# Kernel optimization log

Measured on AMD Instinct MI355X. Metric: run time of the kernel, lower is better.

The kernel has to match this reference:

```python
import jax, jax.numpy as jnp
import numpy as np

D_MODEL = 1024
N_HEAD = 16
D_HEAD = D_MODEL // N_HEAD
SEQ = 1024
RLEN = 2 * SEQ
BATCH = 4
LN_EPS = 1e-5


def setup_inputs() -> dict:
    key = jax.random.key(0)
    ks = jax.random.split(key, 12)
    s = 0.02
    return {
        "h": jax.random.normal(ks[0], (SEQ, BATCH, D_MODEL), jnp.float32),
        "r": jax.random.normal(ks[1], (RLEN, BATCH, D_MODEL), jnp.float32),
        "q_w": jax.random.normal(ks[2], (D_MODEL, N_HEAD, D_HEAD), jnp.float32) * s,
        "k_w": jax.random.normal(ks[3], (D_MODEL, N_HEAD, D_HEAD), jnp.float32) * s,
        "v_w": jax.random.normal(ks[4], (D_MODEL, N_HEAD, D_HEAD), jnp.float32) * s,
        "o_w": jax.random.normal(ks[5], (D_MODEL, N_HEAD, D_HEAD), jnp.float32) * s,
        "r_w": jax.random.normal(ks[6], (D_MODEL, N_HEAD, D_HEAD), jnp.float32) * s,
        "r_r_bias": jax.random.normal(ks[7], (N_HEAD, D_HEAD), jnp.float32) * s,
        "r_w_bias": jax.random.normal(ks[8], (N_HEAD, D_HEAD), jnp.float32) * s,
        "ln_gamma": jnp.ones((D_MODEL,), jnp.float32),
        "ln_beta": jnp.zeros((D_MODEL,), jnp.float32),
    }


def rel_shift_bnij(x, klen):
    # x: [b, n, i, j]; Transformer-XL relative-shift trick
    b, n, i, j = x.shape
    x = x.reshape(b, n, j, i)[:, :, 1:, :].reshape(b, n, i, j - 1)
    return x[:, :, :, :klen]


def reference(h, r, q_w, k_w, v_w, o_w, r_w, r_r_bias, r_w_bias, ln_gamma, ln_beta):
    scale = 1.0 / np.sqrt(D_HEAD).astype(np.float32)
    # projections: i=seq, b=batch, n=heads, d=head dim
    q_head = jnp.einsum('ibh,hnd->ibnd', h, q_w)
    k_head = jnp.einsum('ibh,hnd->ibnd', h, k_w)
    v_head = jnp.einsum('ibh,hnd->ibnd', h, v_w)
    k_head_r = jnp.einsum('ibh,hnd->ibnd', r, r_w)
    # content and position attention scores
    ac = jnp.einsum('ibnd,jbnd->bnij', q_head + r_w_bias, k_head)
    bd = jnp.einsum('ibnd,jbnd->bnij', q_head + r_r_bias, k_head_r)
    bd = rel_shift_bnij(bd, klen=ac.shape[3])
    attn_prob = jax.nn.softmax((ac + bd) * scale, axis=3)  # dropout is identity at eval
    attn_vec = jnp.einsum('bnij,jbnd->ibnd', attn_prob, v_head)
    attn_out = jnp.einsum('ibnd,hnd->ibh', attn_vec, o_w) + h  # residual
    mu = jnp.mean(attn_out, axis=-1, keepdims=True)
    var = jnp.var(attn_out, axis=-1, keepdims=True)
    return (attn_out - mu) / jnp.sqrt(var + LN_EPS) * ln_gamma + ln_beta
```

## Files before the change

### kernel.cpp

```cpp
#include <hip/hip_runtime.h>
#include <stdint.h>


typedef __attribute__((ext_vector_type(8))) short v8s;
typedef __attribute__((ext_vector_type(4))) float v4f;

__device__ __forceinline__ uint16_t f2b(float x) {
    uint32_t u = __builtin_bit_cast(uint32_t, x);
    u += 0x7fffu + ((u >> 16) & 1u);
    return (uint16_t)(u >> 16);
}

__device__ __forceinline__ void gld16(const void* g, void* lds) {
    __builtin_amdgcn_global_load_lds(
        (const __attribute__((address_space(1))) uint32_t*)g,
        (__attribute__((address_space(3))) uint32_t*)lds, 16, 0, 0);
}

__global__ __launch_bounds__(256) void prep_kernel(
    const float* __restrict__ h, const float* __restrict__ r,
    const float* __restrict__ o_w, const float* __restrict__ q_w,
    const float* __restrict__ k_w, const float* __restrict__ v_w,
    const float* __restrict__ r_w,
    uint64_t* __restrict__ hB, uint64_t* __restrict__ rB,
    uint64_t* __restrict__ owB, uint16_t* __restrict__ Wcat,
    uint16_t* __restrict__ rwT)
{
    __shared__ float t[64][65];
    const int bid = blockIdx.x, tid = threadIdx.x;
    if (bid < 1024) {
        const int tx = bid & 15, ty = (bid >> 4) & 15, z = bid >> 8;
        const int n0 = tx * 64, h0 = ty * 64;
        const float* src = (z == 0) ? q_w : (z == 1) ? k_w : (z == 2) ? v_w : r_w;
        uint16_t* dst = (z == 3) ? rwT : Wcat + (size_t)z * 1048576;
#pragma unroll
        for (int q = 0; q < 16; ++q) {
            int idx = q * 256 + tid, rr = idx >> 6, cc = idx & 63;
            t[rr][cc] = src[(size_t)(h0 + rr) * 1024 + n0 + cc];
        }
        __syncthreads();
#pragma unroll
        for (int q = 0; q < 16; ++q) {
            int idx = q * 256 + tid, rr = idx >> 6, cc = idx & 63;
            dst[(size_t)(n0 + rr) * 1024 + h0 + cc] = f2b(t[cc][rr]);
        }
    } else {
        const float4* h4 = (const float4*)h;
        const float4* r4 = (const float4*)r;
        const float4* w4 = (const float4*)o_w;
        const int total = 1048576 + 2097152 + 262144;
        for (int i = (bid - 1024) * 256 + tid; i < total; i += 2048 * 256) {
            float4 v; uint64_t* dst; int idx;
            if (i < 1048576)      { idx = i;           v = h4[idx]; dst = hB; }
            else if (i < 3145728) { idx = i - 1048576; v = r4[idx]; dst = rB; }
            else                  { idx = i - 3145728; v = w4[idx]; dst = owB; }
            uint64_t p = (uint64_t)f2b(v.x) | ((uint64_t)f2b(v.y) << 16)
                       | ((uint64_t)f2b(v.z) << 32) | ((uint64_t)f2b(v.w) << 48);
            dst[idx] = p;
        }
    }
}

template<int MODE, int MI>
__device__ __forceinline__ void gemm_body(
    const uint16_t* __restrict__ A, const uint16_t* __restrict__ B, int K,
    int bx, int by, uint16_t* As, uint16_t* Bs,
    uint16_t* __restrict__ o0, uint16_t* __restrict__ o1,
    uint16_t* __restrict__ o2, uint16_t* __restrict__ o3,
    const float* __restrict__ bias0, const float* __restrict__ bias1,
    float* __restrict__ fo, const float* __restrict__ fres)
{
    const int tid = threadIdx.x;
    const int w = tid >> 6, lane = tid & 63;
    const int g = lane >> 4, c15 = lane & 15;
    const int m0 = by * (MI * 32), n0 = bx * 128;
    const int wr = w >> 1, wc = w & 1;

    int rowA[MI], colA[MI];
#pragma unroll
    for (int q = 0; q < MI; ++q) {
        int D = (w * MI + q) * 1024 + lane * 16;
        int row = D >> 7;
        rowA[q] = row;
        colA[q] = (D & 127) ^ ((row & 7) << 4);
    }
    int rowB[4], colB[4];
#pragma unroll
    for (int q = 0; q < 4; ++q) {
        int D = (w * 4 + q) * 1024 + lane * 16;
        int row = D >> 7;
        rowB[q] = row;
        colB[q] = (D & 127) ^ ((row & 7) << 4);
    }

    v4f acc[MI][4];
#pragma unroll
    for (int i = 0; i < MI; ++i)
#pragma unroll
        for (int j = 0; j < 4; ++j) acc[i][j] = v4f{0.f, 0.f, 0.f, 0.f};

    const char* Abase = (const char*)(A + (size_t)m0 * K);
    const char* Bbase = (const char*)(B + (size_t)n0 * K);
    const size_t ld = (size_t)K * 2;

    for (int kb = 0; kb < K; kb += 64) {
        if (kb) __syncthreads();
#pragma unroll
        for (int q = 0; q < MI; ++q)
            gld16(Abase + (size_t)rowA[q] * ld + (size_t)kb * 2 + colA[q],
                  (char*)As + (w * MI + q) * 1024);
#pragma unroll
        for (int q = 0; q < 4; ++q)
            gld16(Bbase + (size_t)rowB[q] * ld + (size_t)kb * 2 + colB[q],
                  (char*)Bs + (w * 4 + q) * 1024);
        asm volatile("s_waitcnt vmcnt(0)" ::: "memory");
        __syncthreads();

        v8s af[MI][2], bf[4][2];
#pragma unroll
        for (int mi = 0; mi < MI; ++mi) {
            int row = wr * (MI * 16) + mi * 16 + c15;
#pragma unroll
            for (int ks = 0; ks < 2; ++ks) {
                int cl = ks * 64 + g * 16;
                af[mi][ks] = *(const v8s*)((const char*)As + row * 128 + (cl ^ ((row & 7) << 4)));
            }
        }
#pragma unroll
        for (int ni = 0; ni < 4; ++ni) {
            int row = wc * 64 + ni * 16 + c15;
#pragma unroll
            for (int ks = 0; ks < 2; ++ks) {
                int cl = ks * 64 + g * 16;
                bf[ni][ks] = *(const v8s*)((const char*)Bs + row * 128 + (cl ^ ((row & 7) << 4)));
            }
        }
#pragma unroll
        for (int mi = 0; mi < MI; ++mi)
#pragma unroll
            for (int ni = 0; ni < 4; ++ni)
#pragma unroll
                for (int ks = 0; ks < 2; ++ks)
                    acc[mi][ni] = __builtin_amdgcn_mfma_f32_16x16x32_bf16(
                        af[mi][ks], bf[ni][ks], acc[mi][ni], 0, 0, 0);
    }

#pragma unroll
    for (int mi = 0; mi < MI; ++mi)
#pragma unroll
        for (int ni = 0; ni < 4; ++ni)
#pragma unroll
            for (int t = 0; t < 4; ++t) {
                int row = m0 + wr * (MI * 16) + mi * 16 + g * 4 + t;
                int col = n0 + wc * 64 + ni * 16 + c15;
                float v = acc[mi][ni][t];
                if (MODE == 0) {
                    int seg = col >> 10, nd = col & 1023;
                    int i = row >> 2, b = row & 3, n = nd >> 6, d = nd & 63;
                    int bn = b * 16 + n;
                    if (seg == 0) {
                        o0[(bn << 16) + (i << 6) + d] = f2b(v + bias0[nd]);
                        o1[(bn << 16) + (i << 6) + d] = f2b(v + bias1[nd]);
                    } else if (seg == 1) {
                        o2[(bn << 16) + (i << 6) + d] = f2b(v);
                    } else {
                        int il = i & 63;
                        int iperm = (i & ~63) | ((il & 15) * 4 + (il >> 4));
                        o3[(bn << 16) + (d << 10) + iperm] = f2b(v);
                    }
                } else if (MODE == 1) {
                    int j = row >> 2, b = row & 3, n = col >> 6, d = col & 63;
                    int bn = b * 16 + n;
                    o0[(bn << 17) + (j << 6) + d] = f2b(v);
                } else {
                    size_t idx = (size_t)row * 1024 + col;
                    fo[idx] = v + fres[idx];
                }
            }
}

__global__ __launch_bounds__(256) void gemm_qkvr(
    const uint16_t* __restrict__ hB, const uint16_t* __restrict__ Wcat,
    const uint16_t* __restrict__ rB, const uint16_t* __restrict__ rwT,
    uint16_t* __restrict__ Qw, uint16_t* __restrict__ Qr,
    uint16_t* __restrict__ Kt, uint16_t* __restrict__ Vt,
    uint16_t* __restrict__ Kr,
    const float* __restrict__ b0, const float* __restrict__ b1)
{
    __shared__ __align__(16) uint16_t As[128 * 64];
    __shared__ __align__(16) uint16_t Bs[128 * 64];
    const int bid = blockIdx.x;
    if (bid < 768) {
        const int x = bid & 7, l = bid >> 3;
        const int by = (x >> 1) * 8 + l / 12;
        const int bx = (x & 1) * 12 + l % 12;
        gemm_body<0, 4>(hB, Wcat, 1024, bx, by, As, Bs,
                        Qw, Qr, Kt, Vt, b0, b1, nullptr, nullptr);
    } else {
        const int b2 = bid - 768;
        const int x = b2 & 7, l = b2 >> 3;
        const int by = x * 8 + l / 8;
        const int bx = l % 8;
        gemm_body<1, 4>(rB, rwT, 1024, bx, by, As, Bs,
                        Kr, nullptr, nullptr, nullptr, nullptr, nullptr,
                        nullptr, nullptr);
    }
}

__global__ __launch_bounds__(256) void gemm_out(
    const uint16_t* __restrict__ AV, const uint16_t* __restrict__ owB,
    float* __restrict__ AO, const float* __restrict__ hres)
{
    __shared__ __align__(16) uint16_t As[64 * 64];
    __shared__ __align__(16) uint16_t Bs[128 * 64];
    const int x = blockIdx.x & 7, l = blockIdx.x >> 3;
    const int by = x * 8 + l / 8;
    const int bx = l % 8;
    gemm_body<2, 2>(AV, owB, 1024, bx, by, As, Bs,
                    nullptr, nullptr, nullptr, nullptr, nullptr, nullptr,
                    AO, hres);
}

__global__ __launch_bounds__(512, 4) void attn_kernel(
    const uint16_t* __restrict__ Qw, const uint16_t* __restrict__ Qr,
    const uint16_t* __restrict__ Kt, const uint16_t* __restrict__ Vt,
    const uint16_t* __restrict__ Kr, uint16_t* __restrict__ AV)
{
    __shared__ __align__(16) uint16_t Ks[2][4096];
    __shared__ __align__(16) uint16_t Vs[2][4096];
    __shared__ __align__(16) uint16_t Krs[16384];
    __shared__ __align__(16) uint16_t Ptl[8][1024];

    const int tid = threadIdx.x, w = tid >> 6, lane = tid & 63;
    const int g = lane >> 4, c15 = lane & 15;
    const int bid = blockIdx.x;
    const int xcd = bid & 7, slot = bid >> 3;
    const int it = slot & 7, bn = ((slot >> 3) << 3) | xcd;
    const int b = bn >> 4, n = bn & 15;
    const int i0 = it * 128, i0w = i0 + w * 16;
    const int B0 = 897 - i0;

    const uint16_t* qwp = Qw + ((size_t)bn << 16);
    const uint16_t* qrp = Qr + ((size_t)bn << 16);
    const char* ktp = (const char*)(Kt + ((size_t)bn << 16));
    const char* vtp = (const char*)(Vt + ((size_t)bn << 16));
    const char* krp = (const char*)(Kr + ((size_t)bn << 17));

    const int rsub = lane >> 3;
    const int csrc = ((lane & 7) ^ rsub) << 4;
    const int dsto = lane * 16;
    const int swz = (c15 & 7) << 4;

    int sl[4], esel[4];
#pragma unroll
    for (int t = 0; t < 4; ++t) {
        int e = 15 + c15 - (g * 4 + t);
        sl[t] = g * 16 + (e & 15);
        esel[t] = e >> 4;
    }

    v8s qwf[2], qrf[2];
#pragma unroll
    for (int ks = 0; ks < 2; ++ks) {
        qwf[ks] = *(const v8s*)(qwp + ((i0w + c15) << 6) + ks * 32 + g * 8);
        qrf[ks] = *(const v8s*)(qrp + ((i0w + c15) << 6) + ks * 32 + g * 8);
    }

    v4f acc_o[4];
    float psac[4];
#pragma unroll
    for (int df = 0; df < 4; ++df) acc_o[df] = v4f{0.f, 0.f, 0.f, 0.f};
#pragma unroll
    for (int t = 0; t < 4; ++t) psac[t] = 0.f;

    uint16_t* Ptw = Ptl[w];
    const float SCL = 0.18033688f;
    const float MB8 = 11.54156032f;

    gld16(ktp + (size_t)(w * 8 + rsub) * 128 + csrc,
          (char*)Ks[0] + w * 1024 + dsto);
    gld16(vtp + (size_t)(w * 8 + rsub) * 2048 + csrc,
          (char*)Vs[0] + w * 1024 + dsto);
#pragma unroll
    for (int qq = 0; qq < 3; ++qq) {
        const int chunk = qq * 8 + w;
        const int rg = B0 + chunk * 8 + rsub;
        gld16(krp + (size_t)rg * 128 + csrc, (char*)Krs + chunk * 1024 + dsto);
    }
    asm volatile("s_waitcnt vmcnt(0)" ::: "memory");
    __syncthreads();

    for (int jt = 0; jt < 16; ++jt) {
        const int cur = jt & 1;
        if (jt < 15) {
            const int j1 = (jt + 1) * 64;
            gld16(ktp + (size_t)(j1 + w * 8 + rsub) * 128 + csrc,
                  (char*)Ks[cur ^ 1] + w * 1024 + dsto);
            gld16(vtp + (size_t)(w * 8 + rsub) * 2048 + j1 * 2 + csrc,
                  (char*)Vs[cur ^ 1] + w * 1024 + dsto);
            const int sbase = (192 + 64 * jt) & 255;
            int rg = B0 + 192 + 64 * jt + w * 8 + rsub;
            rg = rg > 2047 ? 2047 : rg;
            gld16(krp + (size_t)rg * 128 + csrc,
                  (char*)Krs + (sbase + w * 8) * 128 + dsto);
        }

        v4f ac[4];
#pragma unroll
        for (int jf = 0; jf < 4; ++jf) ac[jf] = v4f{0.f, 0.f, 0.f, 0.f};
        v4f pp[5];
#pragma unroll
        for (int pf = 0; pf < 5; ++pf) pp[pf] = v4f{0.f, 0.f, 0.f, 0.f};

        __builtin_amdgcn_s_setprio(1);
#pragma unroll
        for (int jf = 0; jf < 4; ++jf) {
            const char* krow = (const char*)Ks[cur] + (jf * 16 + c15) * 128;
#pragma unroll
            for (int ks = 0; ks < 2; ++ks) {
                v8s kf = *(const v8s*)(krow + ((ks * 64 + g * 16) ^ swz));
                ac[jf] = __builtin_amdgcn_mfma_f32_16x16x32_bf16(qwf[ks], kf, ac[jf], 0, 0, 0);
            }
        }
        const int krbase = 64 * jt + 112 - 16 * w + c15;
#pragma unroll
        for (int pf = 0; pf < 5; ++pf) {
            const int sltr = (krbase + 16 * pf) & 255;
            const char* krow = (const char*)Krs + sltr * 128;
#pragma unroll
            for (int ks = 0; ks < 2; ++ks) {
                v8s krf = *(const v8s*)(krow + ((ks * 64 + g * 16) ^ swz));
                pp[pf] = __builtin_amdgcn_mfma_f32_16x16x32_bf16(qrf[ks], krf, pp[pf], 0, 0, 0);
            }
        }
        __builtin_amdgcn_s_setprio(0);

        float spp[5][4];
#pragma unroll
        for (int pf = 0; pf < 5; ++pf)
#pragma unroll
            for (int t = 0; t < 4; ++t)
                spp[pf][t] = __shfl(pp[pf][t], sl[t]);

#pragma unroll
        for (int t = 0; t < 4; ++t) {
            float p[4];
#pragma unroll
            for (int jf = 0; jf < 4; ++jf) {
                float bd = esel[t] ? spp[jf + 1][t] : spp[jf][t];
                p[jf] = exp2f((ac[jf][t] + bd) * SCL - MB8);
                psac[t] += p[jf];
            }
            uint32_t w0, w1;
            asm("v_cvt_pk_bf16_f32 %0, %1, %2" : "=v"(w0) : "v"(p[0]), "v"(p[1]));
            asm("v_cvt_pk_bf16_f32 %0, %1, %2" : "=v"(w1) : "v"(p[2]), "v"(p[3]));
            const int rw = g * 4 + t;
            *(uint2*)((char*)Ptw + rw * 128 + ((c15 * 8) ^ ((rw & 7) << 4))) =
                uint2{w0, w1};
        }
        asm volatile("s_waitcnt lgkmcnt(0)" ::: "memory");

        v8s pa[2];
#pragma unroll
        for (int ks = 0; ks < 2; ++ks)
            pa[ks] = *(const v8s*)((const char*)Ptw + c15 * 128 + ((ks * 64 + g * 16) ^ swz));
        __builtin_amdgcn_s_setprio(1);
#pragma unroll
        for (int df = 0; df < 4; ++df) {
            const char* vrow = (const char*)Vs[cur] + (df * 16 + c15) * 128;
#pragma unroll
            for (int ks = 0; ks < 2; ++ks) {
                v8s vf = *(const v8s*)(vrow + ((ks * 64 + g * 16) ^ swz));
                acc_o[df] = __builtin_amdgcn_mfma_f32_16x16x32_bf16(pa[ks], vf, acc_o[df], 0, 0, 0);
            }
        }
        __builtin_amdgcn_s_setprio(0);

        asm volatile("s_waitcnt vmcnt(0)" ::: "memory");
        __syncthreads();
    }

    float rinv[4];
#pragma unroll
    for (int t = 0; t < 4; ++t) {
        float l = psac[t];
#pragma unroll
        for (int m = 1; m < 16; m <<= 1) l += __shfl_xor(l, m);
        rinv[t] = 1.0f / l;
    }
#pragma unroll
    for (int df = 0; df < 4; ++df)
#pragma unroll
        for (int t = 0; t < 4; ++t) {
            int i = i0w + g * 4 + t;
            int d = df * 16 + c15;
            AV[((size_t)(i * 4 + b) << 10) + n * 64 + d] =
                f2b(acc_o[df][t] * rinv[t]);
        }
}

__global__ __launch_bounds__(256) void ln_kernel(
    const float* __restrict__ AO, const float* __restrict__ gamma,
    const float* __restrict__ beta, float* __restrict__ out)
{
    const int w = threadIdx.x >> 6, lane = threadIdx.x & 63;
    const int row = blockIdx.x * 4 + w;
    const float4* src = (const float4*)(AO + (size_t)row * 1024);
    float4 v[4];
    float s = 0.f, sq = 0.f;
#pragma unroll
    for (int q = 0; q < 4; ++q) {
        v[q] = src[lane + q * 64];
        s += v[q].x + v[q].y + v[q].z + v[q].w;
        sq += v[q].x * v[q].x + v[q].y * v[q].y + v[q].z * v[q].z + v[q].w * v[q].w;
    }
#pragma unroll
    for (int m = 1; m < 64; m <<= 1) { s += __shfl_xor(s, m); sq += __shfl_xor(sq, m); }
    float mean = s * (1.f / 1024.f);
    float var = sq * (1.f / 1024.f) - mean * mean;
    float rstd = rsqrtf(var + 1e-5f);
    const float4* g4 = (const float4*)gamma;
    const float4* b4 = (const float4*)beta;
    float4* o4 = (float4*)(out + (size_t)row * 1024);
#pragma unroll
    for (int q = 0; q < 4; ++q) {
        float4 gg = g4[lane + q * 64], bb = b4[lane + q * 64], vv = v[q], r;
        r.x = (vv.x - mean) * rstd * gg.x + bb.x;
        r.y = (vv.y - mean) * rstd * gg.y + bb.y;
        r.z = (vv.z - mean) * rstd * gg.z + bb.z;
        r.w = (vv.w - mean) * rstd * gg.w + bb.w;
        o4[lane + q * 64] = r;
    }
}

extern "C" void kernel_launch(void* const* d_in, const int* in_sizes, int n_in,
                              void* d_out, int out_size, void* d_ws, size_t ws_size,
                              hipStream_t stream)
{
    const float* h        = (const float*)d_in[0];
    const float* r        = (const float*)d_in[1];
    const float* q_w      = (const float*)d_in[2];
    const float* k_w      = (const float*)d_in[3];
    const float* v_w      = (const float*)d_in[4];
    const float* o_w      = (const float*)d_in[5];
    const float* r_w      = (const float*)d_in[6];
    const float* r_r_bias = (const float*)d_in[7];
    const float* r_w_bias = (const float*)d_in[8];
    const float* ln_gamma = (const float*)d_in[9];
    const float* ln_beta  = (const float*)d_in[10];
    float* out = (float*)d_out;

    char* ws = (char*)d_ws;
    const size_t MB = 1u << 20;
    uint16_t* hB   = (uint16_t*)(ws + 0);
    uint16_t* rB   = (uint16_t*)(ws + 8 * MB);
    uint16_t* Wcat = (uint16_t*)(ws + 24 * MB);
    uint16_t* rwT  = (uint16_t*)(ws + 30 * MB);
    uint16_t* owB  = (uint16_t*)(ws + 32 * MB);
    uint16_t* Qw   = (uint16_t*)(ws + 34 * MB);
    uint16_t* Qr   = (uint16_t*)(ws + 42 * MB);
    uint16_t* Kt   = (uint16_t*)(ws + 50 * MB);
    uint16_t* Vt   = (uint16_t*)(ws + 58 * MB);
    uint16_t* Kr   = (uint16_t*)(ws + 66 * MB);
    uint16_t* AV   = hB;
    float*    AO   = (float*)rB;

    prep_kernel<<<3072, 256, 0, stream>>>(h, r, o_w, q_w, k_w, v_w, r_w,
                                          (uint64_t*)hB, (uint64_t*)rB,
                                          (uint64_t*)owB, Wcat, rwT);
    gemm_qkvr<<<1280, 256, 0, stream>>>(hB, Wcat, rB, rwT,
                                        Qw, Qr, Kt, Vt, Kr, r_w_bias, r_r_bias);
    attn_kernel<<<512, 512, 0, stream>>>(Qw, Qr, Kt, Vt, Kr, AV);
    gemm_out<<<512, 256, 0, stream>>>(AV, owB, AO, h);
    ln_kernel<<<1024, 256, 0, stream>>>(AO, ln_gamma, ln_beta, out);
}
```

Before: 153.1 us.

## Give each attention wave two 16-row query tiles to reuse K/V fragments

The attention kernel drops from 8 waves of 16 query rows to 4 waves of 32 query rows per block. Each K, V and Kr fragment read from LDS now feeds two MFMAs, and the positional scores share six Kr tiles across the two row tiles instead of five per tile. This halves LDS fragment reads per MFMA, at the cost of doubled accumulator registers per wave and fewer waves per block to hide latency.

```diff
diff --git a/kernel.cpp b/kernel.cpp
--- a/kernel.cpp
+++ b/kernel.cpp
@@ -221,7 +221,7 @@
                     AO, hres);
 }
 
-__global__ __launch_bounds__(512, 4) void attn_kernel(
+__global__ __launch_bounds__(256, 2) void attn_kernel(
     const uint16_t* __restrict__ Qw, const uint16_t* __restrict__ Qr,
     const uint16_t* __restrict__ Kt, const uint16_t* __restrict__ Vt,
     const uint16_t* __restrict__ Kr, uint16_t* __restrict__ AV)
@@ -229,7 +229,7 @@
     __shared__ __align__(16) uint16_t Ks[2][4096];
     __shared__ __align__(16) uint16_t Vs[2][4096];
     __shared__ __align__(16) uint16_t Krs[16384];
-    __shared__ __align__(16) uint16_t Ptl[8][1024];
+    __shared__ __align__(16) uint16_t Ptl[4][2048];
 
     const int tid = threadIdx.x, w = tid >> 6, lane = tid & 63;
     const int g = lane >> 4, c15 = lane & 15;
@@ -237,7 +237,7 @@
     const int xcd = bid & 7, slot = bid >> 3;
     const int it = slot & 7, bn = ((slot >> 3) << 3) | xcd;
     const int b = bn >> 4, n = bn & 15;
-    const int i0 = it * 128, i0w = i0 + w * 16;
+    const int i0 = it * 128, i0w = i0 + w * 32;
     const int B0 = 897 - i0;
 
     const uint16_t* qwp = Qw + ((size_t)bn << 16);
@@ -259,31 +259,40 @@
         esel[t] = e >> 4;
     }
 
-    v8s qwf[2], qrf[2];
-#pragma unroll
-    for (int ks = 0; ks < 2; ++ks) {
-        qwf[ks] = *(const v8s*)(qwp + ((i0w + c15) << 6) + ks * 32 + g * 8);
-        qrf[ks] = *(const v8s*)(qrp + ((i0w + c15) << 6) + ks * 32 + g * 8);
-    }
-
-    v4f acc_o[4];
-    float psac[4];
-#pragma unroll
-    for (int df = 0; df < 4; ++df) acc_o[df] = v4f{0.f, 0.f, 0.f, 0.f};
-#pragma unroll
-    for (int t = 0; t < 4; ++t) psac[t] = 0.f;
+    v8s qwf[2][2], qrf[2][2];
+#pragma unroll
+    for (int mi = 0; mi < 2; ++mi)
+#pragma unroll
+        for (int ks = 0; ks < 2; ++ks) {
+            qwf[mi][ks] = *(const v8s*)(qwp + ((i0w + mi * 16 + c15) << 6) + ks * 32 + g * 8);
+            qrf[mi][ks] = *(const v8s*)(qrp + ((i0w + mi * 16 + c15) << 6) + ks * 32 + g * 8);
+        }
+
+    v4f acc_o[2][4];
+    float psac[2][4];
+#pragma unroll
+    for (int mi = 0; mi < 2; ++mi)
+#pragma unroll
+        for (int df = 0; df < 4; ++df) {
+            acc_o[mi][df] = v4f{0.f, 0.f, 0.f, 0.f};
+            psac[mi][df] = 0.f;
+        }
 
     uint16_t* Ptw = Ptl[w];
     const float SCL = 0.18033688f;
     const float MB8 = 11.54156032f;
 
-    gld16(ktp + (size_t)(w * 8 + rsub) * 128 + csrc,
-          (char*)Ks[0] + w * 1024 + dsto);
-    gld16(vtp + (size_t)(w * 8 + rsub) * 2048 + csrc,
-          (char*)Vs[0] + w * 1024 + dsto);
-#pragma unroll
-    for (int qq = 0; qq < 3; ++qq) {
-        const int chunk = qq * 8 + w;
+#pragma unroll
+    for (int qq = 0; qq < 2; ++qq) {
+        const int chunk = qq * 4 + w;
+        gld16(ktp + (size_t)(chunk * 8 + rsub) * 128 + csrc,
+              (char*)Ks[0] + chunk * 1024 + dsto);
+        gld16(vtp + (size_t)(chunk * 8 + rsub) * 2048 + csrc,
+              (char*)Vs[0] + chunk * 1024 + dsto);
+    }
+#pragma unroll
+    for (int qq = 0; qq < 6; ++qq) {
+        const int chunk = qq * 4 + w;
         const int rg = B0 + chunk * 8 + rsub;
         gld16(krp + (size_t)rg * 128 + csrc, (char*)Krs + chunk * 1024 + dsto);
     }
@@ -294,23 +303,26 @@
         const int cur = jt & 1;
         if (jt < 15) {
             const int j1 = (jt + 1) * 64;
-            gld16(ktp + (size_t)(j1 + w * 8 + rsub) * 128 + csrc,
-                  (char*)Ks[cur ^ 1] + w * 1024 + dsto);
-            gld16(vtp + (size_t)(w * 8 + rsub) * 2048 + j1 * 2 + csrc,
-                  (char*)Vs[cur ^ 1] + w * 1024 + dsto);
             const int sbase = (192 + 64 * jt) & 255;
-            int rg = B0 + 192 + 64 * jt + w * 8 + rsub;
-            rg = rg > 2047 ? 2047 : rg;
-            gld16(krp + (size_t)rg * 128 + csrc,
-                  (char*)Krs + (sbase + w * 8) * 128 + dsto);
-        }
-
-        v4f ac[4];
-#pragma unroll
-        for (int jf = 0; jf < 4; ++jf) ac[jf] = v4f{0.f, 0.f, 0.f, 0.f};
-        v4f pp[5];
-#pragma unroll
-        for (int pf = 0; pf < 5; ++pf) pp[pf] = v4f{0.f, 0.f, 0.f, 0.f};
+#pragma unroll
+            for (int qq = 0; qq < 2; ++qq) {
+                const int chunk = qq * 4 + w;
+                gld16(ktp + (size_t)(j1 + chunk * 8 + rsub) * 128 + csrc,
+                      (char*)Ks[cur ^ 1] + chunk * 1024 + dsto);
+                gld16(vtp + (size_t)(chunk * 8 + rsub) * 2048 + j1 * 2 + csrc,
+                      (char*)Vs[cur ^ 1] + chunk * 1024 + dsto);
+                int rg = B0 + 192 + 64 * jt + chunk * 8 + rsub;
+                rg = rg > 2047 ? 2047 : rg;
+                gld16(krp + (size_t)rg * 128 + csrc,
+                      (char*)Krs + (sbase + chunk * 8) * 128 + dsto);
+            }
+        }
+
+        v4f ac[2][4];
+#pragma unroll
+        for (int mi = 0; mi < 2; ++mi)
+#pragma unroll
+            for (int jf = 0; jf < 4; ++jf) ac[mi][jf] = v4f{0.f, 0.f, 0.f, 0.f};
 
         __builtin_amdgcn_s_setprio(1);
 #pragma unroll
@@ -319,51 +331,69 @@
 #pragma unroll
             for (int ks = 0; ks < 2; ++ks) {
                 v8s kf = *(const v8s*)(krow + ((ks * 64 + g * 16) ^ swz));
-                ac[jf] = __builtin_amdgcn_mfma_f32_16x16x32_bf16(qwf[ks], kf, ac[jf], 0, 0, 0);
-            }
-        }
-        const int krbase = 64 * jt + 112 - 16 * w + c15;
+                ac[0][jf] = __builtin_amdgcn_mfma_f32_16x16x32_bf16(qwf[0][ks], kf, ac[0][jf], 0, 0, 0);
+                ac[1][jf] = __builtin_amdgcn_mfma_f32_16x16x32_bf16(qwf[1][ks], kf, ac[1][jf], 0, 0, 0);
+            }
+        }
+        v4f pp0[5], pp1[5];
 #pragma unroll
         for (int pf = 0; pf < 5; ++pf) {
+            pp0[pf] = v4f{0.f, 0.f, 0.f, 0.f};
+            pp1[pf] = v4f{0.f, 0.f, 0.f, 0.f};
+        }
+        const int krbase = 64 * jt + 96 - 32 * w + c15;
+#pragma unroll
+        for (int pf = 0; pf < 6; ++pf) {
             const int sltr = (krbase + 16 * pf) & 255;
             const char* krow = (const char*)Krs + sltr * 128;
 #pragma unroll
             for (int ks = 0; ks < 2; ++ks) {
                 v8s krf = *(const v8s*)(krow + ((ks * 64 + g * 16) ^ swz));
-                pp[pf] = __builtin_amdgcn_mfma_f32_16x16x32_bf16(qrf[ks], krf, pp[pf], 0, 0, 0);
+                if (pf >= 1)
+                    pp0[pf - 1] = __builtin_amdgcn_mfma_f32_16x16x32_bf16(qrf[0][ks], krf, pp0[pf - 1], 0, 0, 0);
+                if (pf <= 4)
+                    pp1[pf] = __builtin_amdgcn_mfma_f32_16x16x32_bf16(qrf[1][ks], krf, pp1[pf], 0, 0, 0);
             }
         }
         __builtin_amdgcn_s_setprio(0);
 
-        float spp[5][4];
+        float spp0[5][4], spp1[5][4];
 #pragma unroll
         for (int pf = 0; pf < 5; ++pf)
 #pragma unroll
-            for (int t = 0; t < 4; ++t)
-                spp[pf][t] = __shfl(pp[pf][t], sl[t]);
-
-#pragma unroll
-        for (int t = 0; t < 4; ++t) {
-            float p[4];
-#pragma unroll
-            for (int jf = 0; jf < 4; ++jf) {
-                float bd = esel[t] ? spp[jf + 1][t] : spp[jf][t];
-                p[jf] = exp2f((ac[jf][t] + bd) * SCL - MB8);
-                psac[t] += p[jf];
-            }
-            uint32_t w0, w1;
-            asm("v_cvt_pk_bf16_f32 %0, %1, %2" : "=v"(w0) : "v"(p[0]), "v"(p[1]));
-            asm("v_cvt_pk_bf16_f32 %0, %1, %2" : "=v"(w1) : "v"(p[2]), "v"(p[3]));
-            const int rw = g * 4 + t;
-            *(uint2*)((char*)Ptw + rw * 128 + ((c15 * 8) ^ ((rw & 7) << 4))) =
-                uint2{w0, w1};
+            for (int t = 0; t < 4; ++t) {
+                spp0[pf][t] = __shfl(pp0[pf][t], sl[t]);
+                spp1[pf][t] = __shfl(pp1[pf][t], sl[t]);
+            }
+
+#pragma unroll
+        for (int mi = 0; mi < 2; ++mi) {
+#pragma unroll
+            for (int t = 0; t < 4; ++t) {
+                float p[4];
+#pragma unroll
+                for (int jf = 0; jf < 4; ++jf) {
+                    float bd = mi ? (esel[t] ? spp1[jf + 1][t] : spp1[jf][t])
+                                  : (esel[t] ? spp0[jf + 1][t] : spp0[jf][t]);
+                    p[jf] = exp2f((ac[mi][jf][t] + bd) * SCL - MB8);
+                    psac[mi][t] += p[jf];
+                }
+                uint32_t w0, w1;
+                asm("v_cvt_pk_bf16_f32 %0, %1, %2" : "=v"(w0) : "v"(p[0]), "v"(p[1]));
+                asm("v_cvt_pk_bf16_f32 %0, %1, %2" : "=v"(w1) : "v"(p[2]), "v"(p[3]));
+                const int rw = g * 4 + t;
+                *(uint2*)((char*)Ptw + mi * 2048 + rw * 128 + ((c15 * 8) ^ ((rw & 7) << 4))) =
+                    uint2{w0, w1};
+            }
         }
         asm volatile("s_waitcnt lgkmcnt(0)" ::: "memory");
 
-        v8s pa[2];
-#pragma unroll
-        for (int ks = 0; ks < 2; ++ks)
-            pa[ks] = *(const v8s*)((const char*)Ptw + c15 * 128 + ((ks * 64 + g * 16) ^ swz));
+        v8s pa[2][2];
+#pragma unroll
+        for (int mi = 0; mi < 2; ++mi)
+#pragma unroll
+            for (int ks = 0; ks < 2; ++ks)
+                pa[mi][ks] = *(const v8s*)((const char*)Ptw + mi * 2048 + c15 * 128 + ((ks * 64 + g * 16) ^ swz));
         __builtin_amdgcn_s_setprio(1);
 #pragma unroll
         for (int df = 0; df < 4; ++df) {
@@ -371,7 +401,8 @@
 #pragma unroll
             for (int ks = 0; ks < 2; ++ks) {
                 v8s vf = *(const v8s*)(vrow + ((ks * 64 + g * 16) ^ swz));
-                acc_o[df] = __builtin_amdgcn_mfma_f32_16x16x32_bf16(pa[ks], vf, acc_o[df], 0, 0, 0);
+                acc_o[0][df] = __builtin_amdgcn_mfma_f32_16x16x32_bf16(pa[0][ks], vf, acc_o[0][df], 0, 0, 0);
+                acc_o[1][df] = __builtin_amdgcn_mfma_f32_16x16x32_bf16(pa[1][ks], vf, acc_o[1][df], 0, 0, 0);
             }
         }
         __builtin_amdgcn_s_setprio(0);
@@ -380,23 +411,26 @@
         __syncthreads();
     }
 
-    float rinv[4];
-#pragma unroll
-    for (int t = 0; t < 4; ++t) {
-        float l = psac[t];
-#pragma unroll
-        for (int m = 1; m < 16; m <<= 1) l += __shfl_xor(l, m);
-        rinv[t] = 1.0f / l;
-    }
-#pragma unroll
-    for (int df = 0; df < 4; ++df)
+#pragma unroll
+    for (int mi = 0; mi < 2; ++mi) {
+        float rinv[4];
 #pragma unroll
         for (int t = 0; t < 4; ++t) {
-            int i = i0w + g * 4 + t;
-            int d = df * 16 + c15;
-            AV[((size_t)(i * 4 + b) << 10) + n * 64 + d] =
-                f2b(acc_o[df][t] * rinv[t]);
-        }
+            float l = psac[mi][t];
+#pragma unroll
+            for (int m = 1; m < 16; m <<= 1) l += __shfl_xor(l, m);
+            rinv[t] = 1.0f / l;
+        }
+#pragma unroll
+        for (int df = 0; df < 4; ++df)
+#pragma unroll
+            for (int t = 0; t < 4; ++t) {
+                int i = i0w + mi * 16 + g * 4 + t;
+                int d = df * 16 + c15;
+                AV[((size_t)(i * 4 + b) << 10) + n * 64 + d] =
+                    f2b(acc_o[mi][df][t] * rinv[t]);
+            }
+    }
 }
 
 __global__ __launch_bounds__(256) void ln_kernel(
@@ -470,7 +504,7 @@
                                           (uint64_t*)owB, Wcat, rwT);
     gemm_qkvr<<<1280, 256, 0, stream>>>(hB, Wcat, rB, rwT,
                                         Qw, Qr, Kt, Vt, Kr, r_w_bias, r_r_bias);
-    attn_kernel<<<512, 512, 0, stream>>>(Qw, Qr, Kt, Vt, Kr, AV);
+    attn_kernel<<<512, 256, 0, stream>>>(Qw, Qr, Kt, Vt, Kr, AV);
     gemm_out<<<512, 256, 0, stream>>>(AV, owB, AO, h);
     ln_kernel<<<1024, 256, 0, stream>>>(AO, ln_gamma, ln_beta, out);
 }
```

Measured after the change: 156.0 us. About the same (+1.9%).
